# Kernel tuning notes

Measured on AMD Instinct MI355X. Metric: run time of the kernel, lower is better.

## Reference

```python
import jax, jax.numpy as jnp
import numpy as np

MIN_T = 0.1  # cfg.min_threshold
MAX_T = 0.9  # cfg.max_threshold
L = 2        # cfg.gcn_layers
B, S, D = 8, 1024, 512


def _gcn(x, adj, Ws, bs):
    # Prune/threshold the soft adjacency: keep weights in [MIN_T, MAX_T].
    adj = adj * ((adj >= MIN_T) & (adj <= MAX_T)).astype(adj.dtype)
    denom = jnp.sum(adj, axis=-1, keepdims=True) + 1.0  # +1 for self-loop
    for l in range(Ws.shape[0]):
        Ax = jnp.einsum('bxy,byd->bxd', adj, x)          # aggregate neighbors
        h = jnp.einsum('bxd,de->bxe', Ax + x, Ws[l]) + bs[l]  # self-loop + transform
        x = jax.nn.relu(h / denom)
    return x  # dropout layers are identity in eval mode


def setup_inputs() -> dict:
    key = jax.random.key(0)
    ks = jax.random.split(key, 8)
    seq_encoder_reprs = jax.random.normal(ks[0], (B, S, D), dtype=jnp.float32)
    adj_fw = jax.random.uniform(ks[1], (B, S, S), dtype=jnp.float32)
    s = 1.0 / np.sqrt(D)
    W1 = jax.random.normal(ks[2], (L, D, D), dtype=jnp.float32) * s
    b1 = jnp.zeros((L, D), dtype=jnp.float32)
    W2 = jax.random.normal(ks[3], (L, D, D), dtype=jnp.float32) * s
    b2 = jnp.zeros((L, D), dtype=jnp.float32)
    # Original zero-inits U; use small random values for a non-degenerate reference.
    U = jax.random.normal(ks[4], (1, D + 1, D + 1), dtype=jnp.float32) * 0.02
    return {"seq_encoder_reprs": seq_encoder_reprs, "adj_fw": adj_fw,
            "W1": W1, "b1": b1, "W2": W2, "b2": b2, "U": U}


def reference(seq_encoder_reprs, adj_fw, W1, b1, W2, b2, U):
    h1 = _gcn(seq_encoder_reprs, adj_fw, W1, b1)                 # forward-edge stream
    h2 = _gcn(seq_encoder_reprs, adj_fw.transpose(0, 2, 1), W2, b2)  # backward-edge stream
    r1 = jnp.concatenate([h1, jnp.ones_like(h1[..., :1])], axis=-1)  # [B,S,D+1]
    r2 = jnp.concatenate([h2, jnp.ones_like(h2[..., :1])], axis=-1)
    # 'bxi,oij,byj->boxy' then permute(0,2,3,1) -> [B,S,S,O]
    tmp = jnp.einsum('bxi,oij->boxj', r1, U)
    score = jnp.einsum('boxj,byj->boxy', tmp, r2)
    return score.transpose(0, 2, 3, 1)
```

## Files before the change

### kernel.cpp

```cpp
#include <hip/hip_runtime.h>

#define SS 1024
#define DD 512
#define BATCH 8
#define MIN_T 0.1f
#define MAX_T 0.9f

using half8  = __attribute__((ext_vector_type(8))) _Float16;
using floatx4 = __attribute__((ext_vector_type(4))) float;

typedef const __attribute__((address_space(1))) void gvoid;
typedef __attribute__((address_space(3))) void lvoid;

__global__ void rsum_k(const _Float16* __restrict__ A, float* __restrict__ rden, int rows) {
    int row = blockIdx.x * 4 + (threadIdx.x >> 6);
    if (row >= rows) return;
    int lane = threadIdx.x & 63;
    const _Float16* a = A + (size_t)row * SS;
    float s = 0.f;
#pragma unroll
    for (int r = 0; r < 2; ++r) {
        half8 v = *(const half8*)&a[(lane + 64 * r) * 8];
#pragma unroll
        for (int j = 0; j < 8; ++j) s += (float)v[j];
    }
#pragma unroll
    for (int m = 32; m > 0; m >>= 1) s += __shfl_xor(s, m, 64);
    if (lane == 0) rden[row] = 1.0f / (s + 1.0f);
}

template <typename ST, bool PRUNE, bool DON, bool DOT>
__global__ void prep_k(const ST* __restrict__ src, int sld, long bS,
                       _Float16* __restrict__ dN, int ldN, long bN,
                       _Float16* __restrict__ dT, int ldT, long bT,
                       int srcR, int srcC, int dTR, int dTC) {
    __shared__ float lt[64][65];
    src += (size_t)blockIdx.z * bS;
    int c0 = blockIdx.x * 64, r0 = blockIdx.y * 64;
    int tx = threadIdx.x, ty = threadIdx.y;
#pragma unroll
    for (int it = 0; it < 16; ++it) {
        int r = r0 + ty + it * 4, c = c0 + tx;
        float v = 0.f;
        if (r < srcR && c < srcC) v = (float)src[(size_t)r * sld + c];
        if (PRUNE) v = (v >= MIN_T && v <= MAX_T) ? v : 0.f;
        if (DON) {
            if (r < srcR && c < srcC)
                dN[(size_t)blockIdx.z * bN + (size_t)r * ldN + c] = (_Float16)v;
        }
        if (DOT) lt[tx][ty + it * 4] = v;
    }
    if (DOT) {
        __syncthreads();
#pragma unroll
        for (int it = 0; it < 16; ++it) {
            int tr = c0 + ty + it * 4, tc = r0 + tx;
            if (tr < dTR && tc < dTC)
                dT[(size_t)blockIdx.z * bT + (size_t)tr * ldT + tc] =
                    (_Float16)lt[ty + it * 4][tx];
        }
    }
}

__global__ void wprep_k(const float* __restrict__ W1, const float* __restrict__ W2,
                        const float* __restrict__ U, const float* __restrict__ b1,
                        const float* __restrict__ b2, _Float16* __restrict__ Wcat,
                        _Float16* __restrict__ UT, float* __restrict__ Ubias,
                        float* __restrict__ bcat) {
    __shared__ float lt[64][65];
    const int z = blockIdx.z;
    const float* src;
    _Float16* dT;
    int sld, srcR, srcC, dTR, dTC, ldT;
    if (z < 4) {
        int l = z >> 1, st = z & 1;
        src = (st ? W2 : W1) + (size_t)l * DD * DD;
        sld = DD; srcR = DD; srcC = DD;
        dT = Wcat + (size_t)z * DD * DD; ldT = DD; dTR = DD; dTC = DD;
    } else {
        src = U; sld = 513; srcR = 512; srcC = 513;
        dT = UT; ldT = DD; dTR = 640; dTC = DD;
    }
    int c0 = blockIdx.x * 64, r0 = blockIdx.y * 64;
    int tx = threadIdx.x, ty = threadIdx.y;
#pragma unroll
    for (int it = 0; it < 16; ++it) {
        int r = r0 + ty + it * 4, c = c0 + tx;
        float v = 0.f;
        if (r < srcR && c < srcC) v = src[(size_t)r * sld + c];
        lt[tx][ty + it * 4] = v;
    }
    __syncthreads();
#pragma unroll
    for (int it = 0; it < 16; ++it) {
        int tr = c0 + ty + it * 4, tc = r0 + tx;
        if (tr < dTR && tc < dTC)
            dT[(size_t)tr * ldT + tc] = (_Float16)lt[ty + it * 4][tx];
    }
    if (z == 4 && blockIdx.x == 0 && blockIdx.y == 0) {
        int tid = ty * 64 + tx;
        for (int i = tid; i < 2048; i += 256) {
            int l = i >> 10, st = (i >> 9) & 1, n = i & 511;
            bcat[i] = (st == 0) ? b1[l * 512 + n] : b2[l * 512 + n];
        }
        for (int i = tid; i < 576; i += 256) Ubias[i] = (i < 513) ? U[512 * 513 + i] : 0.f;
    }
}

constexpr int GBM = 128, GBN = 128, GBK = 64;

template <int EPI>
__global__ __launch_bounds__(512, 4) void gemm_k(
    const _Float16* __restrict__ A, const _Float16* __restrict__ B, void* __restrict__ Cv,
    void* __restrict__ Cv2,
    int M, int N, int K, int lda, int ldb, int ldc,
    long bA, long bB, long bC, int zmB,
    const void* __restrict__ e0, int e0ld, long bE0, int zmE,
    const float* __restrict__ e1) {
    __shared__ _Float16 lA[2][GBM * GBK];
    __shared__ _Float16 lB[2][GBN * GBK];

    const int gx = gridDim.x, gy = gridDim.y;
    const int nwg = gx * gy * gridDim.z;
    const int orig = (blockIdx.z * gy + blockIdx.y) * gx + blockIdx.x;
    const int w = (orig & 7) * (nwg >> 3) + (orig >> 3);
    const int bx = w % gx;
    const int wt = w / gx;
    const int by = wt % gy;
    const int z = wt / gy;

    A += (size_t)z * bA;
    B += (size_t)(z & zmB) * bB;
    const int m0 = bx * GBM, n0 = by * GBN;
    const int tid = threadIdx.x;
    const int lane = tid & 63, wv = tid >> 6;
    const int wr = wv >> 2, wc = wv & 3;

    auto stage = [&](int buf, int kt) {
#pragma unroll
        for (int it = 0; it < 2; ++it) {
            int q = it * 512 + tid;
            int r = q >> 3, cp = q & 7, cl = cp ^ (r & 7);
            const _Float16* g = A + (size_t)(m0 + r) * lda + kt + cl * 8;
            __builtin_amdgcn_global_load_lds((gvoid*)g,
                (lvoid*)(&lA[buf][(it * 512 + wv * 64) * 8]), 16, 0, 0);
        }
#pragma unroll
        for (int it = 0; it < 2; ++it) {
            int q = it * 512 + tid;
            int r = q >> 3, cp = q & 7, cl = cp ^ (r & 7);
            const _Float16* g = B + (size_t)(n0 + r) * ldb + kt + cl * 8;
            __builtin_amdgcn_global_load_lds((gvoid*)g,
                (lvoid*)(&lB[buf][(it * 512 + wv * 64) * 8]), 16, 0, 0);
        }
    };

    floatx4 acc[4][2] = {};

    stage(0, 0);
    asm volatile("s_waitcnt vmcnt(0)");
    __syncthreads();
    int cur = 0;
    for (int kt = 0; kt < K; kt += GBK) {
        int nxt = kt + GBK;
        if (nxt < K) stage(cur ^ 1, nxt);
#pragma unroll
        for (int kk = 0; kk < 2; ++kk) {
            half8 af[4], bf[2];
#pragma unroll
            for (int i = 0; i < 4; ++i) {
                int row = wr * 64 + i * 16 + (lane & 15);
                int cl = kk * 4 + (lane >> 4);
                int cp = cl ^ (row & 7);
                af[i] = *(const half8*)&lA[cur][row * 64 + cp * 8];
            }
#pragma unroll
            for (int j = 0; j < 2; ++j) {
                int row = wc * 32 + j * 16 + (lane & 15);
                int cl = kk * 4 + (lane >> 4);
                int cp = cl ^ (row & 7);
                bf[j] = *(const half8*)&lB[cur][row * 64 + cp * 8];
            }
#pragma unroll
            for (int i = 0; i < 4; ++i)
#pragma unroll
                for (int j = 0; j < 2; ++j)
                    acc[i][j] = __builtin_amdgcn_mfma_f32_16x16x32_f16(af[i], bf[j], acc[i][j], 0, 0, 0);
        }
        if (nxt < K) {
            asm volatile("s_waitcnt vmcnt(0)");
            __syncthreads();
        }
        cur ^= 1;
    }

    const int cm = (lane >> 4) * 4;
    const int cn = lane & 15;
    const long bAct = (long)SS * DD;
#pragma unroll
    for (int i = 0; i < 4; ++i) {
#pragma unroll
        for (int j = 0; j < 2; ++j) {
#pragma unroll
            for (int r = 0; r < 4; ++r) {
                int m = m0 + wr * 64 + i * 16 + cm + r;
                int n = n0 + wc * 32 + j * 16 + cn;
                float v = acc[i][j][r];
                if constexpr (EPI == 1) {
                    const _Float16* X = (const _Float16*)e0 + (size_t)(z & zmE) * bE0;
                    v += (float)X[(size_t)m * e0ld + n];
                    ((_Float16*)Cv)[(size_t)z * bC + (size_t)m * ldc + n] = (_Float16)v;
                } else if constexpr (EPI == 2 || EPI == 5) {
                    const float* bb = (const float*)e0 + (size_t)(z & zmE) * bE0;
                    v = (v + bb[n]) * e1[(size_t)z * e0ld + m];
                    v = v > 0.f ? v : 0.f;
                    ((_Float16*)Cv)[(size_t)z * bC + (size_t)m * ldc + n] = (_Float16)v;
                    if constexpr (EPI == 5) {
                        int bt = m >> 10, s = m & 1023;
                        ((_Float16*)Cv2)[(size_t)(z * 8 + bt) * bAct + (size_t)n * SS + s] =
                            (_Float16)v;
                    }
                } else if constexpr (EPI == 3) {
                    if (n < N) {
                        v += ((const float*)e0)[n];
                        ((_Float16*)Cv)[(size_t)z * bC + (size_t)m * ldc + n] = (_Float16)v;
                    }
                } else {
                    const _Float16* tb = (const _Float16*)e0 + (size_t)(z & zmE) * bE0;
                    v += (float)tb[(size_t)m * e0ld];
                    ((float*)Cv)[(size_t)z * bC + (size_t)m * ldc + n] = v;
                }
            }
        }
    }
}

extern "C" void kernel_launch(void* const* d_in, const int* in_sizes, int n_in,
                              void* d_out, int out_size, void* d_ws, size_t ws_size,
                              hipStream_t stream) {
    const float* x0  = (const float*)d_in[0];
    const float* adj = (const float*)d_in[1];
    const float* W1  = (const float*)d_in[2];
    const float* b1  = (const float*)d_in[3];
    const float* W2  = (const float*)d_in[4];
    const float* b2  = (const float*)d_in[5];
    const float* U   = (const float*)d_in[6];
    float* out = (float*)d_out;

    char* ws = (char*)d_ws;
    const size_t MB = 1u << 20;
    const long bAdj = (long)SS * SS, bAct = (long)SS * DD;
    const long DD2 = (long)DD * DD;
    _Float16* adjcat = (_Float16*)(ws);
    _Float16* x0t  = (_Float16*)(ws + 32 * MB);
    _Float16* x0h  = (_Float16*)(ws + 40 * MB);
    _Float16* u1   = (_Float16*)(ws + 48 * MB);
    _Float16* u2   = (_Float16*)(ws + 64 * MB);
    _Float16* u3   = (_Float16*)(ws + 80 * MB);
    _Float16* h12  = (_Float16*)(ws + 96 * MB);
    _Float16* t1h  = (_Float16*)(ws + 112 * MB);
    _Float16* Wcat = (_Float16*)(ws + 122 * MB);
    _Float16* UT   = (_Float16*)(ws + 124 * MB);
    float* Ubias   = (float*)(ws + 125 * MB);
    float* bcat    = (float*)(ws + 125 * MB + 4096);
    float* rden12  = (float*)(ws + 125 * MB + 16384);

    dim3 tb(64, 4);
    wprep_k<<<dim3(10, 8, 5), tb, 0, stream>>>(W1, W2, U, b1, b2, Wcat, UT, Ubias, bcat);
    prep_k<float, false, true, true><<<dim3(8, 16, BATCH), tb, 0, stream>>>(
        x0, DD, bAct, x0h, DD, bAct, x0t, SS, bAct, SS, DD, DD, SS);
    prep_k<float, true, true, true><<<dim3(16, 16, BATCH), tb, 0, stream>>>(
        adj, SS, bAdj, adjcat, SS, bAdj, adjcat + 8 * bAdj, SS, bAdj, SS, SS, SS, SS);
    rsum_k<<<16384 / 4, 256, 0, stream>>>(adjcat, rden12, 16384);

    dim3 gAgg(SS / GBM, DD / GBN, 16);
    dim3 gWmm(BATCH * SS / GBM, DD / GBN, 2);
    dim3 gT1(BATCH * SS / GBM, 5, 1);
    dim3 gSc(SS / GBM, SS / GBN, BATCH);

    gemm_k<1><<<gAgg, 512, 0, stream>>>(adjcat, x0t, u1, nullptr, SS, DD, SS, SS, SS, DD,
                                        bAdj, bAct, bAct, 7, x0h, DD, bAct, 7, nullptr);
    gemm_k<5><<<gWmm, 512, 0, stream>>>(u1, Wcat, u2, u3, BATCH * SS, DD, DD, DD, DD, DD,
                                        8 * bAct, DD2, 8 * bAct, 1,
                                        bcat, 8192, 512, 1, rden12);
    gemm_k<1><<<gAgg, 512, 0, stream>>>(adjcat, u3, u1, nullptr, SS, DD, SS, SS, SS, DD,
                                        bAdj, bAct, bAct, 15, u2, DD, bAct, 15, nullptr);
    gemm_k<2><<<gWmm, 512, 0, stream>>>(u1, Wcat + 2 * DD2, h12, nullptr,
                                        BATCH * SS, DD, DD, DD, DD, DD,
                                        8 * bAct, DD2, 8 * bAct, 1,
                                        bcat + 1024, 8192, 512, 1, rden12);

    gemm_k<3><<<gT1, 512, 0, stream>>>(h12, UT, t1h, nullptr, BATCH * SS, 576, DD, DD, DD, 576,
                                       0, 0, 0, 0, Ubias, 0, 0, 0, nullptr);
    gemm_k<4><<<gSc, 512, 0, stream>>>(t1h, h12 + 8 * bAct, out, nullptr, SS, SS, DD, 576, DD, SS,
                                       (long)SS * 576, bAct, (long)SS * SS, 15,
                                       t1h + 512, 576, (long)SS * 576, 15, nullptr);
}
```

Baseline: 168.4 us.

## Fuse prep kernels into one launch and compute adjacency row sums during pruning

Merges the weight-transpose, activation-convert and adjacency prune/transpose kernels into a single launch whose block ID selects the job. Row and column partial sums of the pruned adjacency are computed inside the prune tile pass and written to a partial buffer, so the old row-sum kernel no longer re-reads the 32MB fp16 adjacency; a small kernel reduces the partials. This cuts launch count and memory traffic, at the cost of extra shuffles in the prune loop and a partial-sum buffer.

Result: faster. 157.2 us (-6.6%).

```diff
diff --git a/kernel.cpp b/kernel.cpp
--- a/kernel.cpp
+++ b/kernel.cpp
@@ -12,99 +12,119 @@
 typedef const __attribute__((address_space(1))) void gvoid;
 typedef __attribute__((address_space(3))) void lvoid;
 
-__global__ void rsum_k(const _Float16* __restrict__ A, float* __restrict__ rden, int rows) {
-    int row = blockIdx.x * 4 + (threadIdx.x >> 6);
-    if (row >= rows) return;
-    int lane = threadIdx.x & 63;
-    const _Float16* a = A + (size_t)row * SS;
-    float s = 0.f;
-#pragma unroll
-    for (int r = 0; r < 2; ++r) {
-        half8 v = *(const half8*)&a[(lane + 64 * r) * 8];
-#pragma unroll
-        for (int j = 0; j < 8; ++j) s += (float)v[j];
-    }
-#pragma unroll
-    for (int m = 32; m > 0; m >>= 1) s += __shfl_xor(s, m, 64);
-    if (lane == 0) rden[row] = 1.0f / (s + 1.0f);
-}
-
-template <typename ST, bool PRUNE, bool DON, bool DOT>
-__global__ void prep_k(const ST* __restrict__ src, int sld, long bS,
-                       _Float16* __restrict__ dN, int ldN, long bN,
-                       _Float16* __restrict__ dT, int ldT, long bT,
-                       int srcR, int srcC, int dTR, int dTC) {
+__global__ void mega_k(const float* __restrict__ x0, const float* __restrict__ adj,
+                       const float* __restrict__ W1, const float* __restrict__ W2,
+                       const float* __restrict__ U, const float* __restrict__ b1,
+                       const float* __restrict__ b2,
+                       _Float16* __restrict__ adjcat, _Float16* __restrict__ x0h,
+                       _Float16* __restrict__ x0t, _Float16* __restrict__ Wcat,
+                       _Float16* __restrict__ UT, float* __restrict__ Ubias,
+                       float* __restrict__ bcat, float* __restrict__ part) {
     __shared__ float lt[64][65];
-    src += (size_t)blockIdx.z * bS;
-    int c0 = blockIdx.x * 64, r0 = blockIdx.y * 64;
-    int tx = threadIdx.x, ty = threadIdx.y;
-#pragma unroll
-    for (int it = 0; it < 16; ++it) {
-        int r = r0 + ty + it * 4, c = c0 + tx;
-        float v = 0.f;
-        if (r < srcR && c < srcC) v = (float)src[(size_t)r * sld + c];
-        if (PRUNE) v = (v >= MIN_T && v <= MAX_T) ? v : 0.f;
-        if (DON) {
-            if (r < srcR && c < srcC)
-                dN[(size_t)blockIdx.z * bN + (size_t)r * ldN + c] = (_Float16)v;
-        }
-        if (DOT) lt[tx][ty + it * 4] = v;
-    }
-    if (DOT) {
+    __shared__ float csum[4][64];
+    const int id = blockIdx.x;
+    const int tx = threadIdx.x, ty = threadIdx.y;
+
+    if (id < 2048) {
+        int z = id >> 8, y = (id >> 4) & 15, x = id & 15;
+        int r0 = y * 64, c0 = x * 64;
+        const float* src = adj + (size_t)z * SS * SS;
+        _Float16* dN = adjcat + (size_t)z * SS * SS;
+        _Float16* dT = adjcat + (size_t)(8 + z) * SS * SS;
+        float colacc = 0.f;
+#pragma unroll
+        for (int it = 0; it < 16; ++it) {
+            int r = r0 + ty + it * 4, c = c0 + tx;
+            float v = src[(size_t)r * SS + c];
+            v = (v >= MIN_T && v <= MAX_T) ? v : 0.f;
+            dN[(size_t)r * SS + c] = (_Float16)v;
+            lt[tx][ty + it * 4] = v;
+            colacc += v;
+            float rs = v;
+#pragma unroll
+            for (int m = 32; m > 0; m >>= 1) rs += __shfl_xor(rs, m, 64);
+            if (tx == 0) part[((size_t)z * SS + r) * 16 + x] = rs;
+        }
+        csum[ty][tx] = colacc;
+        __syncthreads();
+#pragma unroll
+        for (int it = 0; it < 16; ++it) {
+            int tr = c0 + ty + it * 4, tc = r0 + tx;
+            dT[(size_t)tr * SS + tc] = (_Float16)lt[ty + it * 4][tx];
+        }
+        if (ty == 0) {
+            float cs = csum[0][tx] + csum[1][tx] + csum[2][tx] + csum[3][tx];
+            part[(size_t)131072 + ((size_t)z * SS + (c0 + tx)) * 16 + y] = cs;
+        }
+    } else if (id < 3072) {
+        int rel = id - 2048;
+        int z = rel >> 7, y = (rel >> 3) & 15, x = rel & 7;
+        int r0 = y * 64, c0 = x * 64;
+        const float* src = x0 + (size_t)z * SS * DD;
+        _Float16* dN = x0h + (size_t)z * SS * DD;
+        _Float16* dT = x0t + (size_t)z * SS * DD;
+#pragma unroll
+        for (int it = 0; it < 16; ++it) {
+            int r = r0 + ty + it * 4, c = c0 + tx;
+            float v = src[(size_t)r * DD + c];
+            dN[(size_t)r * DD + c] = (_Float16)v;
+            lt[tx][ty + it * 4] = v;
+        }
+        __syncthreads();
+#pragma unroll
+        for (int it = 0; it < 16; ++it) {
+            int tr = c0 + ty + it * 4, tc = r0 + tx;
+            dT[(size_t)tr * SS + tc] = (_Float16)lt[ty + it * 4][tx];
+        }
+    } else {
+        int rel = id - 3072;
+        int z = rel / 80, rem = rel % 80;
+        int y = rem / 10, x = rem % 10;
+        const float* src;
+        _Float16* dT;
+        int sld, srcR, srcC, dTR, dTC, ldT;
+        if (z < 4) {
+            int l = z >> 1, st = z & 1;
+            src = (st ? W2 : W1) + (size_t)l * DD * DD;
+            sld = DD; srcR = DD; srcC = DD;
+            dT = Wcat + (size_t)z * DD * DD; ldT = DD; dTR = DD; dTC = DD;
+        } else {
+            src = U; sld = 513; srcR = 512; srcC = 513;
+            dT = UT; ldT = DD; dTR = 640; dTC = DD;
+        }
+        int c0 = x * 64, r0 = y * 64;
+#pragma unroll
+        for (int it = 0; it < 16; ++it) {
+            int r = r0 + ty + it * 4, c = c0 + tx;
+            float v = 0.f;
+            if (r < srcR && c < srcC) v = src[(size_t)r * sld + c];
+            lt[tx][ty + it * 4] = v;
+        }
         __syncthreads();
 #pragma unroll
         for (int it = 0; it < 16; ++it) {
             int tr = c0 + ty + it * 4, tc = r0 + tx;
             if (tr < dTR && tc < dTC)
-                dT[(size_t)blockIdx.z * bT + (size_t)tr * ldT + tc] =
-                    (_Float16)lt[ty + it * 4][tx];
+                dT[(size_t)tr * ldT + tc] = (_Float16)lt[ty + it * 4][tx];
+        }
+        if (z == 4 && x == 0 && y == 0) {
+            int tid = ty * 64 + tx;
+            for (int i = tid; i < 2048; i += 256) {
+                int l = i >> 10, st = (i >> 9) & 1, n = i & 511;
+                bcat[i] = (st == 0) ? b1[l * 512 + n] : b2[l * 512 + n];
+            }
+            for (int i = tid; i < 576; i += 256) Ubias[i] = (i < 513) ? U[512 * 513 + i] : 0.f;
         }
     }
 }
 
-__global__ void wprep_k(const float* __restrict__ W1, const float* __restrict__ W2,
-                        const float* __restrict__ U, const float* __restrict__ b1,
-                        const float* __restrict__ b2, _Float16* __restrict__ Wcat,
-                        _Float16* __restrict__ UT, float* __restrict__ Ubias,
-                        float* __restrict__ bcat) {
-    __shared__ float lt[64][65];
-    const int z = blockIdx.z;
-    const float* src;
-    _Float16* dT;
-    int sld, srcR, srcC, dTR, dTC, ldT;
-    if (z < 4) {
-        int l = z >> 1, st = z & 1;
-        src = (st ? W2 : W1) + (size_t)l * DD * DD;
-        sld = DD; srcR = DD; srcC = DD;
-        dT = Wcat + (size_t)z * DD * DD; ldT = DD; dTR = DD; dTC = DD;
-    } else {
-        src = U; sld = 513; srcR = 512; srcC = 513;
-        dT = UT; ldT = DD; dTR = 640; dTC = DD;
-    }
-    int c0 = blockIdx.x * 64, r0 = blockIdx.y * 64;
-    int tx = threadIdx.x, ty = threadIdx.y;
-#pragma unroll
-    for (int it = 0; it < 16; ++it) {
-        int r = r0 + ty + it * 4, c = c0 + tx;
-        float v = 0.f;
-        if (r < srcR && c < srcC) v = src[(size_t)r * sld + c];
-        lt[tx][ty + it * 4] = v;
-    }
-    __syncthreads();
-#pragma unroll
-    for (int it = 0; it < 16; ++it) {
-        int tr = c0 + ty + it * 4, tc = r0 + tx;
-        if (tr < dTR && tc < dTC)
-            dT[(size_t)tr * ldT + tc] = (_Float16)lt[ty + it * 4][tx];
-    }
-    if (z == 4 && blockIdx.x == 0 && blockIdx.y == 0) {
-        int tid = ty * 64 + tx;
-        for (int i = tid; i < 2048; i += 256) {
-            int l = i >> 10, st = (i >> 9) & 1, n = i & 511;
-            bcat[i] = (st == 0) ? b1[l * 512 + n] : b2[l * 512 + n];
-        }
-        for (int i = tid; i < 576; i += 256) Ubias[i] = (i < 513) ? U[512 * 513 + i] : 0.f;
-    }
+__global__ void rsum2_k(const float* __restrict__ part, float* __restrict__ rden) {
+    int row = blockIdx.x * 256 + threadIdx.x;
+    const float* p = part + (size_t)row * 16;
+    float s = 0.f;
+#pragma unroll
+    for (int i = 0; i < 16; ++i) s += p[i];
+    rden[row] = 1.0f / (s + 1.0f);
 }
 
 constexpr int GBM = 128, GBN = 128, GBK = 64;
@@ -264,14 +284,11 @@
     float* Ubias   = (float*)(ws + 125 * MB);
     float* bcat    = (float*)(ws + 125 * MB + 4096);
     float* rden12  = (float*)(ws + 125 * MB + 16384);
-
-    dim3 tb(64, 4);
-    wprep_k<<<dim3(10, 8, 5), tb, 0, stream>>>(W1, W2, U, b1, b2, Wcat, UT, Ubias, bcat);
-    prep_k<float, false, true, true><<<dim3(8, 16, BATCH), tb, 0, stream>>>(
-        x0, DD, bAct, x0h, DD, bAct, x0t, SS, bAct, SS, DD, DD, SS);
-    prep_k<float, true, true, true><<<dim3(16, 16, BATCH), tb, 0, stream>>>(
-        adj, SS, bAdj, adjcat, SS, bAdj, adjcat + 8 * bAdj, SS, bAdj, SS, SS, SS, SS);
-    rsum_k<<<16384 / 4, 256, 0, stream>>>(adjcat, rden12, 16384);
+    float* part    = (float*)(ws + 126 * MB);
+
+    mega_k<<<3472, dim3(64, 4), 0, stream>>>(x0, adj, W1, W2, U, b1, b2,
+                                             adjcat, x0h, x0t, Wcat, UT, Ubias, bcat, part);
+    rsum2_k<<<64, 256, 0, stream>>>(part, rden12);
 
     dim3 gAgg(SS / GBM, DD / GBN, 16);
     dim3 gWmm(BATCH * SS / GBM, DD / GBN, 2);
```
